# Optimization experiments

Measured on AMD Instinct MI355X. Metric: run time of the kernel, lower is better.

## Reference

```python
import jax, jax.numpy as jnp
import numpy as np

DIM = 1024
H = 16
DPH = DIM // H  # 64
B, S = 4, 2048


def setup_inputs() -> dict:
    key = jax.random.key(0)
    ks = jax.random.split(key, 9)
    s_in = 1.0 / np.sqrt(DIM)
    s_out = 1.0 / np.sqrt(H * DPH)
    return {
        "x": jax.random.normal(ks[0], (B, S, DIM), dtype=jnp.float32),
        "Wq": jax.random.normal(ks[1], (H, DIM, DPH), dtype=jnp.float32) * s_in,
        "bq": jax.random.normal(ks[2], (H, DPH), dtype=jnp.float32) * 0.01,
        "Wk": jax.random.normal(ks[3], (DIM, DPH), dtype=jnp.float32) * s_in,
        "bk": jax.random.normal(ks[4], (DPH,), dtype=jnp.float32) * 0.01,
        "Wv": jax.random.normal(ks[5], (DIM, DPH), dtype=jnp.float32) * s_in,
        "bv": jax.random.normal(ks[6], (DPH,), dtype=jnp.float32) * 0.01,
        "Wo": jax.random.normal(ks[7], (H * DPH, DIM), dtype=jnp.float32) * s_out,
        "bo": jax.random.normal(ks[8], (DIM,), dtype=jnp.float32) * 0.01,
    }


def reference(x, Wq, bq, Wk, bk, Wv, bv, Wo, bo):
    # Multi-query attention: per-head Q, shared K/V. dropout p=0 -> identity.
    scale = 1.0 / jnp.sqrt(jnp.asarray(DPH, dtype=jnp.float32))
    q = jnp.einsum("bsd,hde->bhse", x, Wq) + bq[None, :, None, :]  # [B,H,S,dph]
    k = jnp.einsum("bsd,de->bse", x, Wk) + bk                      # [B,S,dph]
    v = jnp.einsum("bsd,de->bse", x, Wv) + bv                      # [B,S,dph]
    scores = jnp.einsum("bhse,bte->bhst", q, k) * scale            # [B,H,S,S]
    attn = jax.nn.softmax(scores, axis=-1)
    o = jnp.einsum("bhst,bte->bhse", attn, v)                      # [B,H,S,dph]
    # concat heads in head order along last dim -> [B,S,H*dph]
    o = jnp.transpose(o, (0, 2, 1, 3)).reshape(B, S, H * DPH)
    return jnp.einsum("bsf,fd->bsd", o, Wo) + bo
```

## Files before the change

kernel.cpp:

```cpp
#include <hip/hip_runtime.h>
#include <hip/hip_bf16.h>
#include <hip/hip_fp16.h>


typedef _Float16 f16x8 __attribute__((ext_vector_type(8)));
typedef _Float16 f16x4 __attribute__((ext_vector_type(4)));
typedef _Float16 f16x2 __attribute__((ext_vector_type(2)));
typedef float f32x4 __attribute__((ext_vector_type(4)));
typedef float f32x16 __attribute__((ext_vector_type(16)));

#define MFMA16(a, b, c) __builtin_amdgcn_mfma_f32_16x16x32_f16((a), (b), (c), 0, 0, 0)
#define MFMA32(a, b, c) __builtin_amdgcn_mfma_f32_32x32x16_f16((a), (b), (c), 0, 0, 0)
#define PKRTZ(a, b) __builtin_bit_cast(f16x2, __builtin_amdgcn_cvt_pkrtz((a), (b)))

__device__ __forceinline__ void gll16(const void* g, void* l) {
  __builtin_amdgcn_global_load_lds(
      (__attribute__((address_space(1))) void*)const_cast<void*>(g),
      (__attribute__((address_space(3))) void*)l, 16, 0, 0);
}

__global__ __launch_bounds__(256) void pack_x_kernel(const float* __restrict__ x,
                                                     _Float16* __restrict__ xh) {
  int i = blockIdx.x * 256 + threadIdx.x;
  const float4* s = (const float4*)x + (size_t)i * 2;
  float4 a = s[0], b = s[1];
  f16x8 h;
  h[0] = (_Float16)a.x; h[1] = (_Float16)a.y; h[2] = (_Float16)a.z; h[3] = (_Float16)a.w;
  h[4] = (_Float16)b.x; h[5] = (_Float16)b.y; h[6] = (_Float16)b.z; h[7] = (_Float16)b.w;
  ((f16x8*)xh)[i] = h;
}

__global__ __launch_bounds__(256) void pack_w_kernel(
    const float* __restrict__ Wq, const float* __restrict__ Wk,
    const float* __restrict__ Wv, const float* __restrict__ Wo,
    _Float16* __restrict__ wqkvT, _Float16* __restrict__ woT) {
  int i = blockIdx.x * 256 + threadIdx.x;
  if (i < 1048576) {
    int n = i >> 10, d = i & 1023;
    int h = n >> 6, e = n & 63;
    wqkvT[i] = (_Float16)Wq[h * 65536 + d * 64 + e];
  } else if (i < 1114112) {
    int j = i - 1048576;
    int e = j >> 10, d = j & 1023;
    wqkvT[i] = (_Float16)Wk[d * 64 + e];
  } else if (i < 1179648) {
    int j = i - 1114112;
    int e = j >> 10, d = j & 1023;
    wqkvT[i] = (_Float16)Wv[d * 64 + e];
  } else {
    int j = i - 1179648;
    int d = j >> 10, f = j & 1023;
    woT[j] = (_Float16)Wo[f * 1024 + d];
  }
}

struct GemmAcc {
  f32x4 acc[4][4];
};

__device__ __forceinline__ void gemm128_core(
    const _Float16* __restrict__ A, const _Float16* __restrict__ Bp,
    int m0, int n0, _Float16* abuf, _Float16* bbuf, GemmAcc& g) {
  const int tid = threadIdx.x;
  const int lane = tid & 63, wave = tid >> 6;
  const int wr = wave >> 1, wc = wave & 1;
  const int g4 = lane >> 4, l15 = lane & 15;

  const char* Ag = (const char*)(A + (size_t)m0 * 1024);
  const char* Bg = (const char*)(Bp + (size_t)n0 * 1024);

  const int c0 = tid, c1 = tid + 256;
  const size_t aoff0 = (size_t)(c0 >> 2) * 2048 + (size_t)(c0 & 3) * 16;
  const size_t aoff1 = (size_t)(c1 >> 2) * 2048 + (size_t)(c1 & 3) * 16;
  char* ldsa0 = (char*)abuf + c0 * 16;
  char* ldsa1 = (char*)abuf + c1 * 16;
  char* ldsb0 = (char*)bbuf + c0 * 16;
  char* ldsb1 = (char*)bbuf + c1 * 16;

  const char* ar[4];
  const char* br[4];
  #pragma unroll
  for (int mt = 0; mt < 4; mt++)
    ar[mt] = (const char*)abuf + ((wr << 6) + (mt << 4) + l15) * 64 + (g4 << 4);
  #pragma unroll
  for (int nt = 0; nt < 4; nt++)
    br[nt] = (const char*)bbuf + ((wc << 6) + (nt << 4) + l15) * 64 + (g4 << 4);

  for (int k0 = 0; k0 < 1024; k0 += 32) {
    const size_t kb = (size_t)k0 * 2;
    gll16(Ag + aoff0 + kb, ldsa0);
    gll16(Ag + aoff1 + kb, ldsa1);
    gll16(Bg + aoff0 + kb, ldsb0);
    gll16(Bg + aoff1 + kb, ldsb1);
    __syncthreads();
    f16x8 af[4], bf[4];
    #pragma unroll
    for (int mt = 0; mt < 4; mt++) af[mt] = *(const f16x8*)ar[mt];
    #pragma unroll
    for (int nt = 0; nt < 4; nt++) bf[nt] = *(const f16x8*)br[nt];
    #pragma unroll
    for (int mt = 0; mt < 4; mt++)
      #pragma unroll
      for (int nt = 0; nt < 4; nt++)
        g.acc[mt][nt] = MFMA16(af[mt], bf[nt], g.acc[mt][nt]);
    __syncthreads();
  }
}

__global__ __launch_bounds__(256) void gemm_qkv_kernel(
    const _Float16* __restrict__ xh, const _Float16* __restrict__ wT,
    const float* __restrict__ bq, const float* __restrict__ bk,
    const float* __restrict__ bv,
    _Float16* __restrict__ qh, _Float16* __restrict__ kh,
    _Float16* __restrict__ vth) {
  __shared__ __align__(16) _Float16 abuf[128 * 32];
  __shared__ __align__(16) _Float16 bbuf[128 * 32];
  const int lane = threadIdx.x & 63, wave = threadIdx.x >> 6;
  const int wr = wave >> 1, wc = wave & 1;
  const int g4 = lane >> 4, l15 = lane & 15;
  const int m0 = blockIdx.x * 128;
  const int n0 = blockIdx.y * 128;
  GemmAcc g = {};
  gemm128_core(xh, wT, m0, n0, abuf, bbuf, g);

  const float QSCALE = 0.18033688011112042f;
  #pragma unroll
  for (int mt = 0; mt < 4; mt++) {
    int rbase = m0 + wr * 64 + mt * 16 + (g4 << 2);
    int bb = rbase >> 11;
    int s = rbase & 2047;
    #pragma unroll
    for (int nt = 0; nt < 4; nt++) {
      int n = n0 + wc * 64 + nt * 16 + l15;
      if (n < 1024) {
        float bias = bq[n];
        int h = n >> 6, e = n & 63;
        _Float16* dst = qh + (((size_t)(bb * 16 + h) * 2048 + s) * 64 + e);
        #pragma unroll
        for (int r = 0; r < 4; r++)
          dst[(size_t)r * 64] = (_Float16)((g.acc[mt][nt][r] + bias) * QSCALE);
      } else if (n < 1088) {
        int e = n - 1024;
        float bias = bk[e];
        _Float16* dst = kh + ((size_t)bb * 2048 + s) * 64 + e;
        #pragma unroll
        for (int r = 0; r < 4; r++) dst[(size_t)r * 64] = (_Float16)(g.acc[mt][nt][r] + bias);
      } else {
        int e = n - 1088;
        float bias = bv[e];
        f16x4 t;
        #pragma unroll
        for (int r = 0; r < 4; r++) t[r] = (_Float16)(g.acc[mt][nt][r] + bias);
        *(f16x4*)(vth + ((size_t)bb * 64 + e) * 2048 + s) = t;
      }
    }
  }
}

__global__ __launch_bounds__(256) void gemm_out_kernel(
    const _Float16* __restrict__ oh, const _Float16* __restrict__ woT,
    const float* __restrict__ bo, float* __restrict__ out) {
  __shared__ __align__(16) _Float16 abuf[128 * 32];
  __shared__ __align__(16) _Float16 bbuf[128 * 32];
  const int lane = threadIdx.x & 63, wave = threadIdx.x >> 6;
  const int wr = wave >> 1, wc = wave & 1;
  const int g4 = lane >> 4, l15 = lane & 15;
  const int m0 = blockIdx.x * 128;
  const int n0 = blockIdx.y * 128;
  GemmAcc g = {};
  gemm128_core(oh, woT, m0, n0, abuf, bbuf, g);

  #pragma unroll
  for (int mt = 0; mt < 4; mt++) {
    int rbase = m0 + wr * 64 + mt * 16 + (g4 << 2);
    #pragma unroll
    for (int nt = 0; nt < 4; nt++) {
      int n = n0 + wc * 64 + nt * 16 + l15;
      float bias = bo[n];
      #pragma unroll
      for (int r = 0; r < 4; r++)
        out[(size_t)(rbase + r) * 1024 + n] = g.acc[mt][nt][r] + bias;
    }
  }
}

__global__ __launch_bounds__(512) void attn_kernel(
    const _Float16* __restrict__ qh, const _Float16* __restrict__ kh,
    const _Float16* __restrict__ vth, _Float16* __restrict__ oh) {
  __shared__ __align__(16) _Float16 smem[16384];
  const int tid = threadIdx.x;
  const int lane = tid & 63, wave = tid >> 6;
  const int l31 = lane & 31, h = lane >> 5;
  const int b = blockIdx.z, hd = blockIdx.y;
  const int q0 = blockIdx.x * 256;

  const _Float16* Qrow = qh + (((size_t)(b * 16 + hd) * 2048 + q0 + wave * 32 + l31) * 64);
  f16x8 qf[4];
  #pragma unroll
  for (int s = 0; s < 4; s++) qf[s] = *(const f16x8*)(Qrow + s * 16 + h * 8);

  const char* Kb = (const char*)(kh + (size_t)b * 2048 * 64);
  const char* Vb = (const char*)(vth + (size_t)b * 64 * 2048);

  const char* srcK;
  const char* srcV;
  int dsto;
  {
    int c = tid;
    int m = c >> 3, c8 = c & 7;
    int gc = c8 ^ (m & 7);
    int tsrc = (m & 51) | ((m & 4) << 1) | ((m & 8) >> 1);
    srcK = Kb + (size_t)tsrc * 128 + gc * 16;
    srcV = Vb + (size_t)m * 4096 + gc * 16;
    dsto = c * 16;
  }
  char* const ldsb = (char*)smem;

  const int swz = l31 & 7;
  int ro[4][2];
  #pragma unroll
  for (int s = 0; s < 4; s++) {
    int ch = ((2 * s + h) ^ swz) << 4;
    ro[s][0] = l31 * 128 + ch;
    ro[s][1] = (l31 + 32) * 128 + ch;
  }

  float negm = 0.f, l_run = 0.f;
  f32x16 oa0 = {}, oa1 = {};
  const f16x2 one2 = {(_Float16)1.0f, (_Float16)1.0f};

  auto STAGE = [&](int t, int buf) {
    gll16(srcK + (size_t)t * 8192, ldsb + buf * 8192 + dsto);
    gll16(srcV + (size_t)t * 128, ldsb + 16384 + buf * 8192 + dsto);
  };

  STAGE(0, 0);
  __syncthreads();

  for (int it = 0; it < 32; ++it) {
    const int cur = it & 1;
    const char* kb = ldsb + cur * 8192;
    const char* vb = kb + 16384;

    if (it + 1 < 32) STAGE(it + 1, cur ^ 1);

    f32x16 s0, s1;
    #pragma unroll
    for (int i = 0; i < 16; i++) { s0[i] = negm; s1[i] = negm; }
    #pragma unroll
    for (int s = 0; s < 4; s++) {
      f16x8 a0 = *(const f16x8*)(kb + ro[s][0]);
      f16x8 a1 = *(const f16x8*)(kb + ro[s][1]);
      s0 = MFMA32(a0, qf[s], s0);
      s1 = MFMA32(a1, qf[s], s1);
    }

    float vm[8];
    #pragma unroll
    for (int i = 0; i < 8; i++)
      vm[i] = fmaxf(fmaxf(s0[i], s0[i + 8]), fmaxf(s1[i], s1[i + 8]));
    float pm = fmaxf(fmaxf(fmaxf(vm[0], vm[1]), fmaxf(vm[2], vm[3])),
                     fmaxf(fmaxf(vm[4], vm[5]), fmaxf(vm[6], vm[7])));
    pm = fmaxf(pm, __shfl_xor(pm, 32));

    if (__any(pm > 8.0f)) {
      float delta = fmaxf(pm, 0.f);
      float al = __builtin_amdgcn_exp2f(-delta);
      l_run *= al;
      oa0 *= al;
      oa1 *= al;
      negm -= delta;
      #pragma unroll
      for (int i = 0; i < 16; i++) { s0[i] -= delta; s1[i] -= delta; }
    }

    #pragma unroll
    for (int i = 0; i < 16; i++) {
      s0[i] = __builtin_amdgcn_exp2f(s0[i]);
      s1[i] = __builtin_amdgcn_exp2f(s1[i]);
    }

    f16x2 pp[16];
    #pragma unroll
    for (int j = 0; j < 8; j++) pp[j] = PKRTZ(s0[2 * j], s0[2 * j + 1]);
    #pragma unroll
    for (int j = 0; j < 8; j++) pp[8 + j] = PKRTZ(s1[2 * j], s1[2 * j + 1]);

    float ps0 = 0.f, ps1 = 0.f, ps2 = 0.f, ps3 = 0.f;
    #pragma unroll
    for (int j = 0; j < 4; j++) {
      ps0 = __builtin_amdgcn_fdot2(pp[j], one2, ps0, false);
      ps1 = __builtin_amdgcn_fdot2(pp[4 + j], one2, ps1, false);
      ps2 = __builtin_amdgcn_fdot2(pp[8 + j], one2, ps2, false);
      ps3 = __builtin_amdgcn_fdot2(pp[12 + j], one2, ps3, false);
    }
    l_run += (ps0 + ps1) + (ps2 + ps3);

    f16x8 pf[4];
    #pragma unroll
    for (int s = 0; s < 4; s++) {
      f16x4 lo = __builtin_shufflevector(pp[s * 4], pp[s * 4 + 1], 0, 1, 2, 3);
      f16x4 hi = __builtin_shufflevector(pp[s * 4 + 2], pp[s * 4 + 3], 0, 1, 2, 3);
      pf[s] = __builtin_shufflevector(lo, hi, 0, 1, 2, 3, 4, 5, 6, 7);
    }

    #pragma unroll
    for (int s = 0; s < 4; s++) {
      f16x8 v0 = *(const f16x8*)(vb + ro[s][0]);
      f16x8 v1 = *(const f16x8*)(vb + ro[s][1]);
      oa0 = MFMA32(v0, pf[s], oa0);
      oa1 = MFMA32(v1, pf[s], oa1);
    }

    __syncthreads();
  }

  l_run += __shfl_xor(l_run, 32);
  _Float16* ob = smem + wave * 2048;
  float invl = 1.0f / l_run;
  #pragma unroll
  for (int rh = 0; rh < 4; rh++) {
    f16x4 t0, t1;
    #pragma unroll
    for (int j = 0; j < 4; j++) {
      t0[j] = (_Float16)(oa0[rh * 4 + j] * invl);
      t1[j] = (_Float16)(oa1[rh * 4 + j] * invl);
    }
    *(f16x4*)&ob[l31 * 64 + ((rh ^ swz) * 8) + h * 4] = t0;
    *(f16x4*)&ob[l31 * 64 + (((rh + 4) ^ swz) * 8) + h * 4] = t1;
  }
  const int q_ = lane >> 1, hf = lane & 1;
  const size_t orow = ((size_t)b * 2048 + q0 + wave * 32 + q_) * 1024 + hd * 64 + hf * 32;
  #pragma unroll
  for (int c = 0; c < 4; c++) {
    f16x8 v = *(const f16x8*)&ob[q_ * 64 + (((hf * 4 + c) ^ (q_ & 7)) * 8)];
    *(f16x8*)(oh + orow + c * 8) = v;
  }
}

extern "C" void kernel_launch(void* const* d_in, const int* in_sizes, int n_in,
                              void* d_out, int out_size, void* d_ws, size_t ws_size,
                              hipStream_t stream) {
  const float* x  = (const float*)d_in[0];
  const float* Wq = (const float*)d_in[1];
  const float* bq = (const float*)d_in[2];
  const float* Wk = (const float*)d_in[3];
  const float* bk = (const float*)d_in[4];
  const float* Wv = (const float*)d_in[5];
  const float* bv = (const float*)d_in[6];
  const float* Wo = (const float*)d_in[7];
  const float* bo = (const float*)d_in[8];
  float* out = (float*)d_out;
  char* ws = (char*)d_ws;

  _Float16* xh   = (_Float16*)(ws);
  _Float16* wqkv = (_Float16*)(ws + 16777216);
  _Float16* woT  = (_Float16*)(ws + 19136512);
  _Float16* qh   = (_Float16*)(ws + 21233664);
  _Float16* kh   = (_Float16*)(ws + 38010880);
  _Float16* vth  = (_Float16*)(ws + 39059456);
  _Float16* oh   = (_Float16*)(ws + 40108032);

  pack_x_kernel<<<4096, 256, 0, stream>>>(x, xh);
  pack_w_kernel<<<8704, 256, 0, stream>>>(Wq, Wk, Wv, Wo, wqkv, woT);
  gemm_qkv_kernel<<<dim3(64, 9), 256, 0, stream>>>(xh, wqkv, bq, bk, bv, qh, kh, vth);
  attn_kernel<<<dim3(8, 16, 4), 512, 0, stream>>>(qh, kh, vth, oh);
  gemm_out_kernel<<<dim3(64, 8), 256, 0, stream>>>(oh, woT, bo, out);
}
```

Before: 168.8 us.

## Double attention block to 1024 threads and merge the pack kernels

The attention kernel now uses 1024-thread blocks that each cover 512 queries, so every staged K/V tile is reused by twice as many query waves. The staging work is split so the first 512 threads load K and the other 512 load V, one load each per iteration. The x and weight fp16 pack kernels are merged into one launch to cut a kernel launch. In exchange, the declared shared memory doubles even though the buffer offsets still use the original 32 KB. The grid also shrinks to 256 large blocks, which may hurt latency hiding and tail balance.

```diff
diff --git a/kernel.cpp b/kernel.cpp
--- a/kernel.cpp
+++ b/kernel.cpp
@@ -19,22 +19,24 @@
       (__attribute__((address_space(3))) void*)l, 16, 0, 0);
 }
 
-__global__ __launch_bounds__(256) void pack_x_kernel(const float* __restrict__ x,
-                                                     _Float16* __restrict__ xh) {
-  int i = blockIdx.x * 256 + threadIdx.x;
-  const float4* s = (const float4*)x + (size_t)i * 2;
-  float4 a = s[0], b = s[1];
-  f16x8 h;
-  h[0] = (_Float16)a.x; h[1] = (_Float16)a.y; h[2] = (_Float16)a.z; h[3] = (_Float16)a.w;
-  h[4] = (_Float16)b.x; h[5] = (_Float16)b.y; h[6] = (_Float16)b.z; h[7] = (_Float16)b.w;
-  ((f16x8*)xh)[i] = h;
-}
-
-__global__ __launch_bounds__(256) void pack_w_kernel(
-    const float* __restrict__ Wq, const float* __restrict__ Wk,
-    const float* __restrict__ Wv, const float* __restrict__ Wo,
-    _Float16* __restrict__ wqkvT, _Float16* __restrict__ woT) {
-  int i = blockIdx.x * 256 + threadIdx.x;
+__global__ __launch_bounds__(256) void pack_all_kernel(
+    const float* __restrict__ x, const float* __restrict__ Wq,
+    const float* __restrict__ Wk, const float* __restrict__ Wv,
+    const float* __restrict__ Wo,
+    _Float16* __restrict__ xh, _Float16* __restrict__ wqkvT,
+    _Float16* __restrict__ woT) {
+  int bid = blockIdx.x;
+  if (bid < 4096) {
+    int i = bid * 256 + threadIdx.x;
+    const float4* s = (const float4*)x + (size_t)i * 2;
+    float4 a = s[0], b = s[1];
+    f16x8 h;
+    h[0] = (_Float16)a.x; h[1] = (_Float16)a.y; h[2] = (_Float16)a.z; h[3] = (_Float16)a.w;
+    h[4] = (_Float16)b.x; h[5] = (_Float16)b.y; h[6] = (_Float16)b.z; h[7] = (_Float16)b.w;
+    ((f16x8*)xh)[i] = h;
+    return;
+  }
+  int i = (bid - 4096) * 256 + threadIdx.x;
   if (i < 1048576) {
     int n = i >> 10, d = i & 1023;
     int h = n >> 6, e = n & 63;
@@ -184,15 +186,15 @@
   }
 }
 
-__global__ __launch_bounds__(512) void attn_kernel(
+__global__ __launch_bounds__(1024) void attn_kernel(
     const _Float16* __restrict__ qh, const _Float16* __restrict__ kh,
     const _Float16* __restrict__ vth, _Float16* __restrict__ oh) {
-  __shared__ __align__(16) _Float16 smem[16384];
+  __shared__ __align__(16) _Float16 smem[32768];
   const int tid = threadIdx.x;
   const int lane = tid & 63, wave = tid >> 6;
   const int l31 = lane & 31, h = lane >> 5;
   const int b = blockIdx.z, hd = blockIdx.y;
-  const int q0 = blockIdx.x * 256;
+  const int q0 = blockIdx.x * 512;
 
   const _Float16* Qrow = qh + (((size_t)(b * 16 + hd) * 2048 + q0 + wave * 32 + l31) * 64);
   f16x8 qf[4];
@@ -202,19 +204,24 @@
   const char* Kb = (const char*)(kh + (size_t)b * 2048 * 64);
   const char* Vb = (const char*)(vth + (size_t)b * 64 * 2048);
 
-  const char* srcK;
-  const char* srcV;
-  int dsto;
+  const bool isK = tid < 512;
+  const char* src;
+  int dstbase;
   {
-    int c = tid;
+    int c = isK ? tid : (tid - 512);
     int m = c >> 3, c8 = c & 7;
     int gc = c8 ^ (m & 7);
-    int tsrc = (m & 51) | ((m & 4) << 1) | ((m & 8) >> 1);
-    srcK = Kb + (size_t)tsrc * 128 + gc * 16;
-    srcV = Vb + (size_t)m * 4096 + gc * 16;
-    dsto = c * 16;
+    if (isK) {
+      int tsrc = (m & 51) | ((m & 4) << 1) | ((m & 8) >> 1);
+      src = Kb + (size_t)tsrc * 128 + gc * 16;
+      dstbase = c * 16;
+    } else {
+      src = Vb + (size_t)m * 4096 + gc * 16;
+      dstbase = 16384 + c * 16;
+    }
   }
   char* const ldsb = (char*)smem;
+  const size_t srcstep = isK ? 8192 : 128;
 
   const int swz = l31 & 7;
   int ro[4][2];
@@ -230,8 +237,7 @@
   const f16x2 one2 = {(_Float16)1.0f, (_Float16)1.0f};
 
   auto STAGE = [&](int t, int buf) {
-    gll16(srcK + (size_t)t * 8192, ldsb + buf * 8192 + dsto);
-    gll16(srcV + (size_t)t * 128, ldsb + 16384 + buf * 8192 + dsto);
+    gll16(src + (size_t)t * srcstep, ldsb + buf * 8192 + dstbase);
   };
 
   STAGE(0, 0);
@@ -361,9 +367,8 @@
   _Float16* vth  = (_Float16*)(ws + 39059456);
   _Float16* oh   = (_Float16*)(ws + 40108032);
 
-  pack_x_kernel<<<4096, 256, 0, stream>>>(x, xh);
-  pack_w_kernel<<<8704, 256, 0, stream>>>(Wq, Wk, Wv, Wo, wqkv, woT);
+  pack_all_kernel<<<12800, 256, 0, stream>>>(x, Wq, Wk, Wv, Wo, xh, wqkv, woT);
   gemm_qkv_kernel<<<dim3(64, 9), 256, 0, stream>>>(xh, wqkv, bq, bk, bv, qh, kh, vth);
-  attn_kernel<<<dim3(8, 16, 4), 512, 0, stream>>>(qh, kh, vth, oh);
+  attn_kernel<<<dim3(4, 16, 4), 1024, 0, stream>>>(qh, kh, vth, oh);
   gemm_out_kernel<<<dim3(64, 8), 256, 0, stream>>>(oh, woT, bo, out);
 }
```

After: 161.2 us (median of 2 runs). -4.5%, faster.
